# Performance work log

Hardware: AMD Instinct MI355X
Metric: run time of the kernel (lower is better)

The kernel has to match this reference:

```python
import jax, jax.numpy as jnp
import numpy as np


def setup_inputs() -> dict:
    key = jax.random.key(0)
    k1, k2, k3, k4 = jax.random.split(key, 4)
    T, B, D_in, D_out = 512, 128, 512, 512
    X = jax.random.normal(k1, (T, B, D_in), dtype=jnp.float32)
    # torch nn.Linear default init: U(-1/sqrt(fan_in), 1/sqrt(fan_in))
    lim_in = 1.0 / np.sqrt(D_in)
    lim_h = 1.0 / np.sqrt(D_out)
    W_in = jax.random.uniform(k2, (D_out, D_in), jnp.float32, -lim_in, lim_in)
    W_h = jax.random.uniform(k3, (D_out, D_out), jnp.float32, -lim_h, lim_h)
    b_h = jax.random.uniform(k4, (D_out,), jnp.float32, -lim_h, lim_h)
    return {"X": X, "W_in": W_in, "W_h": W_h, "b_h": b_h}


def reference(X, W_in, W_h, b_h):
    # X: [T, B, D_in]. h_{t+1} = sigmoid(x_t @ W_in^T + h_t @ W_h^T + b_h)
    B = X.shape[1]
    D_out = W_h.shape[0]
    # Precompute all input projections in one big GEMM (same math).
    Xproj = jnp.einsum('tbi,oi->tbo', X, W_in)  # [T, B, D_out]
    h0 = jnp.zeros((B, D_out), dtype=X.dtype)

    def step(h, xp):
        h_new = jax.nn.sigmoid(xp + h @ W_h.T + b_h)
        return h_new, None

    h_last, _ = jax.lax.scan(step, h0, Xproj)
    return h_last
```

## Files before the change

kernel.cpp:

```cpp
#include <hip/hip_runtime.h>
#include <hip/hip_bf16.h>
#include <stdint.h>

typedef _Float16 f16;
typedef _Float16 f16x2 __attribute__((ext_vector_type(2)));
typedef _Float16 f16x4 __attribute__((ext_vector_type(4)));
typedef _Float16 f16x8 __attribute__((ext_vector_type(8)));
typedef float f32x4 __attribute__((ext_vector_type(4)));
typedef int   i32x4 __attribute__((ext_vector_type(4)));

#define T_STEPS 512
#define BATCH   128
#define DD      512
#define LOG2E   1.44269504088896f

#define XP_OFF  0
#define WF_OFF  (67108864)
#define WHQ_OFF (67108864 + 524288)
#define SC_OFF  (67108864 + 524288 + 262144)

__device__ __forceinline__ f16x2 pk(float a, float b) {
    return __builtin_bit_cast(f16x2, __builtin_amdgcn_cvt_pkrtz(a, b));
}

__device__ __forceinline__ float fast_exp2(float x) {
#if __has_builtin(__builtin_amdgcn_exp2f)
    return __builtin_amdgcn_exp2f(x);
#else
    return exp2f(x);
#endif
}

__device__ __forceinline__ float fast_rcp(float x) {
#if __has_builtin(__builtin_amdgcn_rcpf)
    return __builtin_amdgcn_rcpf(x);
#else
    return 1.0f / x;
#endif
}

__device__ __forceinline__ uint32_t pack_u8(float s, int pos, uint32_t old) {
#if __has_builtin(__builtin_amdgcn_cvt_pk_u8_f32)
    return __builtin_amdgcn_cvt_pk_u8_f32(s, pos, old);
#else
    return old | (((uint32_t)(int)s & 0xFF) << (8 * pos));
#endif
}

#define GLDS(g, l) __builtin_amdgcn_global_load_lds(                               \
        (const __attribute__((address_space(1))) void*)(g),                        \
        (__attribute__((address_space(3))) void*)(l), 16, 0, 0)

__global__ __launch_bounds__(256) void prep_kernel(
        const float* __restrict__ Win, f16* __restrict__ Wf) {
    int idx = blockIdx.x * 256 + threadIdx.x;
    if (idx < 262144) Wf[idx] = (f16)Win[idx];
}

__global__ __launch_bounds__(64) void quant_kernel(
        const float* __restrict__ Wh, char* __restrict__ Whq, float* __restrict__ scales) {
    const int o = blockIdx.x, t = threadIdx.x;
    const float* row = Wh + (size_t)o * 512;
    float v[8];
    float m = 0.f;
#pragma unroll
    for (int j = 0; j < 8; j++) { v[j] = row[t * 8 + j]; m = fmaxf(m, fabsf(v[j])); }
#pragma unroll
    for (int off = 32; off > 0; off >>= 1) m = fmaxf(m, __shfl_xor(m, off));
    if (t == 0) scales[o] = -LOG2E * m * (1.0f / (127.0f * 127.0f));
    const float inv = 127.0f / m;
    const int rt = o >> 4, rl = o & 15;
    const int k0 = t * 8;
    const int ks = k0 >> 6, qq = (k0 >> 4) & 3, j0 = k0 & 15;
    const int l = qq * 16 + rl;
    char* dst = Whq + ((size_t)((rt * 8 + ks) * 64 + l)) * 16 + j0;
#pragma unroll
    for (int j = 0; j < 8; j++) dst[j] = (char)rintf(v[j] * inv);
}

__global__ __launch_bounds__(512, 4) void gemm_kernel(
        const float* __restrict__ X, const f16* __restrict__ Wf,
        const float* __restrict__ bias, f16* __restrict__ Xp) {
    const int tid = threadIdx.x;
    const int l = tid & 63, w = tid >> 6;
    const int q = l >> 4, rl = l & 15;
    const int wm = w >> 2, wn = w & 3;
    const int blk = blockIdx.x;
    const int xcd = blk & 7, kk = blk >> 3;
    const int m_blk = (xcd * 64 + (kk >> 1)) * 128;
    const int n_blk = (kk & 1) * 256;

    __shared__ __align__(16) float As[2][128 * 32];
    __shared__ __align__(16) f16   Bs[2][256 * 32];

    const float* aSrc[2];
#pragma unroll
    for (int c = 0; c < 2; c++)
        aSrc[c] = X + (size_t)(m_blk + w * 16 + c * 8 + (l >> 3)) * 512
                    + (((l & 7) ^ (l >> 3)) << 2);
    const f16* bSrc[2];
#pragma unroll
    for (int c = 0; c < 2; c++)
        bSrc[c] = Wf + (size_t)(n_blk + w * 32 + c * 16 + (l >> 2)) * 512
                     + (((l & 3) ^ ((l >> 3) & 3)) << 3);

    f32x4 acc[4][4] = {};
    const int swA0 = (((2 * q)     ^ (rl & 7)) << 2);
    const int swA1 = (((2 * q + 1) ^ (rl & 7)) << 2);
    const int swB  = ((q ^ ((rl >> 1) & 3)) << 3);

#pragma unroll
    for (int c = 0; c < 2; c++) GLDS(aSrc[c], &As[0][(w * 16 + c * 8) * 32]);
#pragma unroll
    for (int c = 0; c < 2; c++) GLDS(bSrc[c], &Bs[0][(w * 32 + c * 16) * 32]);

    for (int t = 0; t < 16; ++t) {
        const int cur = t & 1;
        __syncthreads();
        if (t < 15) {
            const int kf = (t + 1) * 32;
#pragma unroll
            for (int c = 0; c < 2; c++) GLDS(aSrc[c] + kf, &As[cur ^ 1][(w * 16 + c * 8) * 32]);
#pragma unroll
            for (int c = 0; c < 2; c++) GLDS(bSrc[c] + kf, &Bs[cur ^ 1][(w * 32 + c * 16) * 32]);
        }
        f16x8 af4[4], bf4[4];
#pragma unroll
        for (int i = 0; i < 4; i++) {
            const int row = wm * 64 + i * 16 + rl;
            const float4 h0 = *(const float4*)&As[cur][row * 32 + swA0];
            const float4 h1 = *(const float4*)&As[cur][row * 32 + swA1];
            f16x2 p0 = pk(h0.x, h0.y), p1 = pk(h0.z, h0.w);
            f16x2 p2 = pk(h1.x, h1.y), p3 = pk(h1.z, h1.w);
            f16x8 tv;
            tv[0] = p0[0]; tv[1] = p0[1]; tv[2] = p1[0]; tv[3] = p1[1];
            tv[4] = p2[0]; tv[5] = p2[1]; tv[6] = p3[0]; tv[7] = p3[1];
            af4[i] = tv;
        }
#pragma unroll
        for (int j = 0; j < 4; j++) {
            const int row = wn * 64 + j * 16 + rl;
            bf4[j] = *(const f16x8*)&Bs[cur][row * 32 + swB];
        }
#pragma unroll
        for (int i = 0; i < 4; i++)
#pragma unroll
            for (int j = 0; j < 4; j++)
                acc[i][j] = __builtin_amdgcn_mfma_f32_16x16x32_f16(bf4[j], af4[i], acc[i][j], 0, 0, 0);
    }
#pragma unroll
    for (int j = 0; j < 4; j++) {
        const float4 b4 = *(const float4*)&bias[n_blk + wn * 64 + j * 16 + q * 4];
        const float bb[4] = {b4.x, b4.y, b4.z, b4.w};
#pragma unroll
        for (int i = 0; i < 4; i++) {
            const int m = m_blk + wm * 64 + i * 16 + rl;
            f16x4 v;
#pragma unroll
            for (int r = 0; r < 4; r++)
                v[r] = (f16)(-LOG2E * (acc[i][j][r] + bb[r]));
            *(f16x4*)(Xp + (size_t)m * 512 + n_blk + wn * 64 + j * 16 + q * 4) = v;
        }
    }
}

__global__ __launch_bounds__(1024) void rnn_kernel(
        const char* __restrict__ Whq, const float* __restrict__ scales,
        const f16* __restrict__ Xp, float* __restrict__ out) {
    const int wg = blockIdx.x;
    const int tid = threadIdx.x;
    const int l = tid & 63, w = tid >> 6;
    const int bl = l & 15;
    const int q = l >> 4;
    const int b = wg * 16 + bl;

    __shared__ __align__(16) uint32_t hT[2][2048];

    i32x4 af[2][8];
    {
        const i32x4* wp = (const i32x4*)Whq;
#pragma unroll
        for (int mt = 0; mt < 2; mt++)
#pragma unroll
            for (int ks = 0; ks < 8; ks++)
                af[mt][ks] = wp[((w * 2 + mt) * 8 + ks) * 64 + l];
    }
    float sc[2][4];
#pragma unroll
    for (int mt = 0; mt < 2; mt++)
#pragma unroll
        for (int r = 0; r < 4; r++)
            sc[mt][r] = scales[w * 32 + mt * 16 + q * 4 + r];

    for (int i = tid; i < 2048; i += 1024) hT[0][i] = 0u;
    __syncthreads();

    const f16* xpb = Xp + (size_t)b * 512 + w * 32 + q * 4;
    f16x4 xn0 = *(const f16x4*)(xpb);
    f16x4 xn1 = *(const f16x4*)(xpb + 16);

    const float K127 = 1.0f / 127.0f;
    for (int t = 0; t < T_STEPS; t++) {
        f16x4 xc0 = xn0, xc1 = xn1;
        const size_t tn = (size_t)(t < T_STEPS - 1 ? t + 1 : t) * (BATCH * 512);
        xn0 = *(const f16x4*)(xpb + tn);
        xn1 = *(const f16x4*)(xpb + tn + 16);

        const int rb = t & 1;
        const uint32_t* hrow = &hT[rb][l * 4];
        uint32_t* hwr = &hT[1 - rb][w * 128 + bl * 4 + q];

        i32x4 acc0 = {};
        __builtin_amdgcn_s_setprio(1);
#pragma unroll
        for (int ks = 0; ks < 8; ks++) {
            i32x4 bfr = *(const i32x4*)(hrow + ks * 256);
            acc0 = __builtin_amdgcn_mfma_i32_16x16x64_i8(af[0][ks], bfr, acc0, 0, 0, 0);
        }
        __builtin_amdgcn_s_setprio(0);

        uint32_t pk0 = 0;
#pragma unroll
        for (int r = 0; r < 4; r++) {
            float tt = fmaf((float)acc0[r], sc[0][r], (float)xc0[r]);
            float e  = fast_exp2(tt);
            float eq = fmaf(e, K127, K127);
            float sg = fast_rcp(eq) + 0.5f;
            pk0 = pack_u8(sg, r, pk0);
        }
        hwr[0] = pk0;

        i32x4 acc1 = {};
        __builtin_amdgcn_s_setprio(1);
#pragma unroll
        for (int ks = 0; ks < 8; ks++) {
            i32x4 bfr = *(const i32x4*)(hrow + ks * 256);
            acc1 = __builtin_amdgcn_mfma_i32_16x16x64_i8(af[1][ks], bfr, acc1, 0, 0, 0);
        }
        __builtin_amdgcn_s_setprio(0);

        uint32_t pk1 = 0;
#pragma unroll
        for (int r = 0; r < 4; r++) {
            float tt = fmaf((float)acc1[r], sc[1][r], (float)xc1[r]);
            float e  = fast_exp2(tt);
            float eq = fmaf(e, K127, K127);
            float sg = fast_rcp(eq) + 0.5f;
            pk1 = pack_u8(sg, r, pk1);
        }
        hwr[64] = pk1;
        __syncthreads();
    }
#pragma unroll
    for (int mt = 0; mt < 2; mt++) {
        uint32_t pkq = hT[T_STEPS & 1][w * 128 + mt * 64 + bl * 4 + q];
        float4 o;
        o.x = (float)((pkq      ) & 0xFF) * K127;
        o.y = (float)((pkq >>  8) & 0xFF) * K127;
        o.z = (float)((pkq >> 16) & 0xFF) * K127;
        o.w = (float)((pkq >> 24) & 0xFF) * K127;
        *(float4*)(out + (size_t)b * 512 + w * 32 + mt * 16 + q * 4) = o;
    }
}

extern "C" void kernel_launch(void* const* d_in, const int* in_sizes, int n_in,
                              void* d_out, int out_size, void* d_ws, size_t ws_size,
                              hipStream_t stream) {
    const float* X   = (const float*)d_in[0];
    const float* Win = (const float*)d_in[1];
    const float* Wh  = (const float*)d_in[2];
    const float* bh  = (const float*)d_in[3];
    float* out = (float*)d_out;
    char* ws = (char*)d_ws;
    f16* Xp      = (f16*)(ws + XP_OFF);
    f16* Wf      = (f16*)(ws + WF_OFF);
    char* Whq    = (char*)(ws + WHQ_OFF);
    float* Sc    = (float*)(ws + SC_OFF);

    prep_kernel<<<1024, 256, 0, stream>>>(Win, Wf);
    quant_kernel<<<512, 64, 0, stream>>>(Wh, Whq, Sc);
    gemm_kernel<<<1024, 512, 0, stream>>>(X, Wf, bh, Xp);
    rnn_kernel<<<8, 1024, 0, stream>>>(Whq, Sc, Xp, out);
}
```

Before: 738.1 us.

## Triple-buffer GEMM loads with vmcnt waits and interleave RNN MFMA chains

The input-projection GEMM moves from a double-buffered LDS pipeline with __syncthreads to a three-stage ring. It uses explicit s_waitcnt vmcnt and raw barriers, and lowers the occupancy hint in launch_bounds from 4 to 2 to fit the larger LDS footprint. The B-tile load mapping changes so each wave loads rows at c*128 + w*16. In the recurrent kernel the two MFMA accumulation chains are interleaved in one loop and the setprio hints are dropped, so the two independent chains can hide each other's MFMA latency; the sigmoid epilogue then runs once for both tiles afterward. The trade-off is fewer resident GEMM blocks, and the epilogue no longer overlaps with the second MFMA chain.

```diff
diff --git a/kernel.cpp b/kernel.cpp
--- a/kernel.cpp
+++ b/kernel.cpp
@@ -78,7 +78,7 @@
     for (int j = 0; j < 8; j++) dst[j] = (char)rintf(v[j] * inv);
 }
 
-__global__ __launch_bounds__(512, 4) void gemm_kernel(
+__global__ __launch_bounds__(512, 2) void gemm_kernel(
         const float* __restrict__ X, const f16* __restrict__ Wf,
         const float* __restrict__ bias, f16* __restrict__ Xp) {
     const int tid = threadIdx.x;
@@ -86,12 +86,12 @@
     const int q = l >> 4, rl = l & 15;
     const int wm = w >> 2, wn = w & 3;
     const int blk = blockIdx.x;
-    const int xcd = blk & 7, kk = blk >> 3;
-    const int m_blk = (xcd * 64 + (kk >> 1)) * 128;
-    const int n_blk = (kk & 1) * 256;
-
-    __shared__ __align__(16) float As[2][128 * 32];
-    __shared__ __align__(16) f16   Bs[2][256 * 32];
+    const int xcd = blk & 7, idx = blk >> 3;
+    const int m_blk = (xcd * 64 + (idx >> 1)) * 128;
+    const int n_blk = (idx & 1) * 256;
+
+    __shared__ __align__(16) float As[3][128 * 32];
+    __shared__ __align__(16) f16   Bs[3][256 * 32];
 
     const float* aSrc[2];
 #pragma unroll
@@ -101,29 +101,33 @@
     const f16* bSrc[2];
 #pragma unroll
     for (int c = 0; c < 2; c++)
-        bSrc[c] = Wf + (size_t)(n_blk + w * 32 + c * 16 + (l >> 2)) * 512
+        bSrc[c] = Wf + (size_t)(n_blk + c * 128 + w * 16 + (l >> 2)) * 512
                      + (((l & 3) ^ ((l >> 3) & 3)) << 3);
+
+#define STAGE(kt, sel) do {                                                        \
+        const int kf_ = (kt) * 32;                                                 \
+        GLDS(aSrc[0] + kf_, &As[sel][(w * 16 + 0) * 32]);                          \
+        GLDS(aSrc[1] + kf_, &As[sel][(w * 16 + 8) * 32]);                          \
+        GLDS(bSrc[0] + kf_, &Bs[sel][(0 * 128 + w * 16) * 32]);                    \
+        GLDS(bSrc[1] + kf_, &Bs[sel][(1 * 128 + w * 16) * 32]);                    \
+    } while (0)
 
     f32x4 acc[4][4] = {};
     const int swA0 = (((2 * q)     ^ (rl & 7)) << 2);
     const int swA1 = (((2 * q + 1) ^ (rl & 7)) << 2);
     const int swB  = ((q ^ ((rl >> 1) & 3)) << 3);
 
-#pragma unroll
-    for (int c = 0; c < 2; c++) GLDS(aSrc[c], &As[0][(w * 16 + c * 8) * 32]);
-#pragma unroll
-    for (int c = 0; c < 2; c++) GLDS(bSrc[c], &Bs[0][(w * 32 + c * 16) * 32]);
-
+    STAGE(0, 0);
+    STAGE(1, 1);
+
+#pragma unroll
     for (int t = 0; t < 16; ++t) {
-        const int cur = t & 1;
-        __syncthreads();
-        if (t < 15) {
-            const int kf = (t + 1) * 32;
-#pragma unroll
-            for (int c = 0; c < 2; c++) GLDS(aSrc[c] + kf, &As[cur ^ 1][(w * 16 + c * 8) * 32]);
-#pragma unroll
-            for (int c = 0; c < 2; c++) GLDS(bSrc[c] + kf, &Bs[cur ^ 1][(w * 32 + c * 16) * 32]);
-        }
+        const int cur = t % 3;
+        if (t < 15) asm volatile("s_waitcnt vmcnt(4)" ::: "memory");
+        else        asm volatile("s_waitcnt vmcnt(0)" ::: "memory");
+        __builtin_amdgcn_s_barrier();
+        if (t + 2 < 16) STAGE(t + 2, (t + 2) % 3);
+
         f16x8 af4[4], bf4[4];
 #pragma unroll
         for (int i = 0; i < 4; i++) {
@@ -148,6 +152,7 @@
             for (int j = 0; j < 4; j++)
                 acc[i][j] = __builtin_amdgcn_mfma_f32_16x16x32_f16(bf4[j], af4[i], acc[i][j], 0, 0, 0);
     }
+#undef STAGE
 #pragma unroll
     for (int j = 0; j < 4; j++) {
         const float4 b4 = *(const float4*)&bias[n_blk + wn * 64 + j * 16 + q * 4];
@@ -207,53 +212,32 @@
         xn1 = *(const f16x4*)(xpb + tn + 16);
 
         const int rb = t & 1;
+        i32x4 acc[2] = {};
         const uint32_t* hrow = &hT[rb][l * 4];
-        uint32_t* hwr = &hT[1 - rb][w * 128 + bl * 4 + q];
-
-        i32x4 acc0 = {};
-        __builtin_amdgcn_s_setprio(1);
 #pragma unroll
         for (int ks = 0; ks < 8; ks++) {
             i32x4 bfr = *(const i32x4*)(hrow + ks * 256);
-            acc0 = __builtin_amdgcn_mfma_i32_16x16x64_i8(af[0][ks], bfr, acc0, 0, 0, 0);
-        }
-        __builtin_amdgcn_s_setprio(0);
-
-        uint32_t pk0 = 0;
-#pragma unroll
-        for (int r = 0; r < 4; r++) {
-            float tt = fmaf((float)acc0[r], sc[0][r], (float)xc0[r]);
-            float e  = fast_exp2(tt);
-            float eq = fmaf(e, K127, K127);
-            float sg = fast_rcp(eq) + 0.5f;
-            pk0 = pack_u8(sg, r, pk0);
-        }
-        hwr[0] = pk0;
-
-        i32x4 acc1 = {};
-        __builtin_amdgcn_s_setprio(1);
-#pragma unroll
-        for (int ks = 0; ks < 8; ks++) {
-            i32x4 bfr = *(const i32x4*)(hrow + ks * 256);
-            acc1 = __builtin_amdgcn_mfma_i32_16x16x64_i8(af[1][ks], bfr, acc1, 0, 0, 0);
-        }
-        __builtin_amdgcn_s_setprio(0);
-
-        uint32_t pk1 = 0;
-#pragma unroll
-        for (int r = 0; r < 4; r++) {
-            float tt = fmaf((float)acc1[r], sc[1][r], (float)xc1[r]);
-            float e  = fast_exp2(tt);
-            float eq = fmaf(e, K127, K127);
-            float sg = fast_rcp(eq) + 0.5f;
-            pk1 = pack_u8(sg, r, pk1);
-        }
-        hwr[64] = pk1;
+            acc[0] = __builtin_amdgcn_mfma_i32_16x16x64_i8(af[0][ks], bfr, acc[0], 0, 0, 0);
+            acc[1] = __builtin_amdgcn_mfma_i32_16x16x64_i8(af[1][ks], bfr, acc[1], 0, 0, 0);
+        }
+#pragma unroll
+        for (int mt = 0; mt < 2; mt++) {
+            uint32_t pkq = 0;
+#pragma unroll
+            for (int r = 0; r < 4; r++) {
+                float tt = fmaf((float)acc[mt][r], sc[mt][r], (float)(mt == 0 ? xc0[r] : xc1[r]));
+                float e  = fast_exp2(tt);
+                float eq = fmaf(e, K127, K127);
+                float sg = fast_rcp(eq) + 0.5f;
+                pkq = pack_u8(sg, r, pkq);
+            }
+            hT[1 - rb][(w * 2 + mt) * 64 + bl * 4 + q] = pkq;
+        }
         __syncthreads();
     }
 #pragma unroll
     for (int mt = 0; mt < 2; mt++) {
-        uint32_t pkq = hT[T_STEPS & 1][w * 128 + mt * 64 + bl * 4 + q];
+        uint32_t pkq = hT[T_STEPS & 1][(w * 2 + mt) * 64 + bl * 4 + q];
         float4 o;
         o.x = (float)((pkq      ) & 0xFF) * K127;
         o.y = (float)((pkq >>  8) & 0xFF) * K127;
```

Result: faster. 700.9 us (-5.0%).
